# Optimization experiments

Measured on AMD Instinct MI355X. Metric: run time of the kernel, lower is better.

## Reference

```python
import jax, jax.numpy as jnp
import numpy as np

L, B, E, H, NH = 128, 32, 128, 256, 8
NUM_NODE, ETA = 20000, 100


def setup_inputs() -> dict:
    key = jax.random.key(0)
    ks = jax.random.split(key, 24)
    s = 0.05
    rn = lambda k, sh: jax.random.normal(k, sh, dtype=jnp.float32) * s
    return {
        "node": jax.random.randint(ks[0], (L, B), 0, NUM_NODE + 1),
        "ts": jax.random.normal(ks[1], (L, B, 2), dtype=jnp.float32),
        "seq_lengths": jnp.sort(jax.random.randint(ks[2], (B,), 64, L + 1))[::-1],
        "embed_table": rn(ks[3], (NUM_NODE + 1, E)),
        "Wih0": rn(ks[4], (3 * H, E + 2)), "Whh0": rn(ks[5], (3 * H, H)),
        "bih0": rn(ks[6], (3 * H,)), "bhh0": rn(ks[7], (3 * H,)),
        "Wih1": rn(ks[8], (3 * H, H)), "Whh1": rn(ks[9], (3 * H, H)),
        "bih1": rn(ks[10], (3 * H,)), "bhh1": rn(ks[11], (3 * H,)),
        "Wa0": rn(ks[12], (E, 2 * E)), "ba0": rn(ks[13], (E,)),
        "Wa1": rn(ks[14], (NH, E)), "ba1": rn(ks[15], (NH,)),
        "Wf0": rn(ks[16], (168, H * (NH + 1))), "bf0": rn(ks[17], (168,)),
        "Wf1": rn(ks[18], (ETA, 168)), "bf1": rn(ks[19], (ETA,)),
    }


def gru_layer(x, Wih, Whh, bih, bhh, lengths):
    # x: [L, B, in]; PyTorch GRU cell, with pack/pad semantics:
    # hidden frozen and output zeroed for t >= length (emulates pack_padded_sequence).
    Lx, Bx, _ = x.shape

    def step(h, xs):
        x_t, t = xs
        gi = x_t @ Wih.T + bih          # [B, 3H]
        gh = h @ Whh.T + bhh            # [B, 3H]
        ir, iz, in_ = jnp.split(gi, 3, axis=-1)
        hr, hz, hn = jnp.split(gh, 3, axis=-1)
        r = jax.nn.sigmoid(ir + hr)
        z = jax.nn.sigmoid(iz + hz)
        n = jnp.tanh(in_ + r * hn)
        h_new = (1.0 - z) * n + z * h
        valid = (t < lengths)[:, None]
        h = jnp.where(valid, h_new, h)
        return h, jnp.where(valid, h_new, jnp.zeros_like(h_new))

    h0 = jnp.zeros((Bx, Whh.shape[1]), x.dtype)
    hT, outs = jax.lax.scan(step, h0, (x, jnp.arange(Lx)))
    return outs, hT


def reference(node, ts, seq_lengths, embed_table,
              Wih0, Whh0, bih0, bhh0, Wih1, Whh1, bih1, bhh1,
              Wa0, ba0, Wa1, ba1, Wf0, bf0, Wf1, bf1):
    e = embed_table[node]                          # [L, B, E]
    embeds = jnp.concatenate([e, ts], axis=-1)     # [L, B, E+2]

    # pairwise attention: a[i,j] = e[j], b[i,j] = e[i] (repeat + transpose)
    a = jnp.broadcast_to(e[None], (L, L, B, E))
    b = jnp.broadcast_to(e[:, None], (L, L, B, E))
    pair = jnp.concatenate([a, b], axis=-1)        # [L, L, B, 2E]
    hid = jax.nn.relu(pair @ Wa0.T + ba0)          # [L, L, B, E]
    w = (hid @ Wa1.T + ba1).sum(axis=1)            # [L, B, NH]

    # multiplicative length mask, then softmax over time axis (as in original)
    mask = (jnp.arange(L)[:, None] < seq_lengths[None, :]).astype(w.dtype)[..., None]
    w = jax.nn.softmax(w * mask, axis=0)           # [L, B, NH]

    out0, _ = gru_layer(embeds, Wih0, Whh0, bih0, bhh0, seq_lengths)
    out1, hT = gru_layer(out0, Wih1, Whh1, bih1, bhh1, seq_lengths)  # [L,B,H], [B,H]

    ctx = jnp.einsum('lbh,lbd->bhd', w, out1).reshape(B, NH * H)     # [B, NH*H]
    z = jnp.concatenate([ctx, hT], axis=-1) @ Wf0.T + bf0
    z = jax.nn.selu(z)
    logits = z @ Wf1.T + bf1
    return jax.nn.log_softmax(logits, axis=-1)
```

## Files before the change

kernel.cpp:

```cpp
#include <hip/hip_runtime.h>
#include <hip/hip_bf16.h>

#define LL 128
#define BB 32
#define EE 128
#define HH 256
#define NHH 8
#define G3 768
#define IN0 130
#define ETA 100
#define F1 168
#define CLSIN 2304

typedef _Float16 half_t;
typedef __attribute__((ext_vector_type(2))) _Float16 half2v;
typedef __attribute__((ext_vector_type(8))) _Float16 f16x8;
typedef __attribute__((ext_vector_type(4))) float f32x4;

#if defined(__has_builtin)
#if __has_builtin(__builtin_amdgcn_fdot2)
#define HAVE_FDOT2 1
#endif
#endif

__device__ __forceinline__ float fdot2f(half2v a, half2v b, float c) {
#ifdef HAVE_FDOT2
  return __builtin_amdgcn_fdot2(a, b, c, false);
#else
  return c + (float)a.x * (float)b.x + (float)a.y * (float)b.y;
#endif
}

#define BARRIER_LDS() __asm__ volatile("s_waitcnt lgkmcnt(0)\n\ts_barrier" ::: "memory")

__device__ __forceinline__ float sigmoidf_(float x) { return 1.0f / (1.0f + __expf(-x)); }
__device__ __forceinline__ float tanhf_(float x) { return 1.0f - 2.0f / (__expf(2.0f * x) + 1.0f); }

__global__ void prep_kernel(
    const float* __restrict__ Wa0, const float* __restrict__ Wih0,
    const float* __restrict__ Wih1, const float* __restrict__ Whh0,
    const float* __restrict__ Whh1,
    half_t* __restrict__ Wa0Ta, half_t* __restrict__ Wa0Tb,
    half2v* __restrict__ Wih0T2, half2v* __restrict__ Wih1T2,
    half_t* __restrict__ Whh0h, half_t* __restrict__ Whh1h)
{
  int idx = blockIdx.x * blockDim.x + threadIdx.x;
  const int n1 = 16384, n2 = 16384, n3 = 65 * 768, n4 = 128 * 768, n5 = 196608;
  if (idx < n1) {
    int d = idx >> 7, k = idx & 127;
    Wa0Ta[idx] = (half_t)Wa0[k * 256 + d];
  } else if ((idx -= n1) < n2) {
    int d = idx >> 7, k = idx & 127;
    Wa0Tb[idx] = (half_t)Wa0[k * 256 + 128 + d];
  } else if ((idx -= n2) < n3) {
    int d2 = idx / 768, r = idx % 768;
    half2v w; w.x = (half_t)Wih0[r * IN0 + 2 * d2]; w.y = (half_t)Wih0[r * IN0 + 2 * d2 + 1];
    Wih0T2[idx] = w;
  } else if ((idx -= n3) < n4) {
    int d2 = idx / 768, r = idx % 768;
    half2v w; w.x = (half_t)Wih1[r * HH + 2 * d2]; w.y = (half_t)Wih1[r * HH + 2 * d2 + 1];
    Wih1T2[idx] = w;
  } else if ((idx -= n4) < n5) {
    Whh0h[idx] = (half_t)Whh0[idx];
  } else if ((idx -= n5) < n5) {
    Whh1h[idx] = (half_t)Whh1[idx];
  }
}

__global__ void embed_uv_kernel(
    const int* __restrict__ node,
    const float* __restrict__ table,
    const half_t* __restrict__ Wa0Ta,
    const half_t* __restrict__ Wa0Tb,
    const float* __restrict__ ba0,
    half2v* __restrict__ e_h2,
    float* __restrict__ U,
    float* __restrict__ V)
{
  int lb = blockIdx.x;
  int k = threadIdx.x;
  __shared__ float es[EE];
  int n = node[lb];
  float ev = table[(size_t)n * EE + k];
  es[k] = ev;
  __syncthreads();
  if (k < 64) {
    half2v p; p.x = (half_t)es[2 * k]; p.y = (half_t)es[2 * k + 1];
    e_h2[(size_t)lb * 64 + k] = p;
  }
  float u = 0.f, v = ba0[k];
  #pragma unroll 8
  for (int d = 0; d < EE; ++d) {
    float x = es[d];
    u += (float)Wa0Ta[d * EE + k] * x;
    v += (float)Wa0Tb[d * EE + k] * x;
  }
  U[(size_t)lb * EE + k] = u;
  V[(size_t)lb * EE + k] = v;
}

__global__ __launch_bounds__(128) void attn_w_kernel(
    const float* __restrict__ U, const float* __restrict__ V,
    const float* __restrict__ Wa1,
    const float* __restrict__ ba1,
    float* __restrict__ wpre)
{
  int ig = blockIdx.x >> 5;
  int b = blockIdx.x & 31;
  int i0 = ig * 4;
  int k = threadIdx.x;
  float vk[4];
  #pragma unroll
  for (int ii = 0; ii < 4; ++ii) vk[ii] = V[((size_t)(i0 + ii) * BB + b) * EE + k];
  float wa[NHH], acc[4][NHH];
  #pragma unroll
  for (int h = 0; h < NHH; ++h) wa[h] = Wa1[h * EE + k];
  #pragma unroll
  for (int ii = 0; ii < 4; ++ii)
    #pragma unroll
    for (int h = 0; h < NHH; ++h) acc[ii][h] = 0.f;
  for (int j = 0; j < LL; ++j) {
    float u = U[((size_t)j * BB + b) * EE + k];
    #pragma unroll
    for (int ii = 0; ii < 4; ++ii) {
      float tv = fmaxf(u + vk[ii], 0.f);
      #pragma unroll
      for (int h = 0; h < NHH; ++h) acc[ii][h] += wa[h] * tv;
    }
  }
  __shared__ float part[2][32];
  int wave = k >> 6, lane = k & 63;
  #pragma unroll
  for (int ii = 0; ii < 4; ++ii)
    #pragma unroll
    for (int h = 0; h < NHH; ++h) {
      float a = acc[ii][h];
      #pragma unroll
      for (int off = 32; off > 0; off >>= 1) a += __shfl_xor(a, off, 64);
      if (lane == 0) part[wave][ii * 8 + h] = a;
    }
  __syncthreads();
  if (k < 32) {
    int ii = k >> 3, h = k & 7;
    float w = part[0][k] + part[1][k] + (float)LL * ba1[h];
    wpre[((size_t)(i0 + ii) * BB + b) * NHH + h] = w;
  }
}

__global__ void attn_softmax_kernel(
    const float* __restrict__ wpre, const int* __restrict__ slen,
    float* __restrict__ wsoft)
{
  int b = blockIdx.x >> 3;
  int h = blockIdx.x & 7;
  int l = threadIdx.x;
  int len = slen[b];
  float x = wpre[((size_t)l * BB + b) * NHH + h];
  float xv = (l < len) ? x : 0.f;
  float m = xv;
  #pragma unroll
  for (int off = 32; off > 0; off >>= 1) m = fmaxf(m, __shfl_xor(m, off, 64));
  __shared__ float sm[2], ss[2];
  int wave = l >> 6;
  if ((l & 63) == 0) sm[wave] = m;
  __syncthreads();
  m = fmaxf(sm[0], sm[1]);
  float e = __expf(xv - m);
  float s = e;
  #pragma unroll
  for (int off = 32; off > 0; off >>= 1) s += __shfl_xor(s, off, 64);
  if ((l & 63) == 0) ss[wave] = s;
  __syncthreads();
  s = ss[0] + ss[1];
  wsoft[((size_t)l * BB + b) * NHH + h] = e / s;
}

__global__ __launch_bounds__(256) void gi0_kernel(
    const half2v* __restrict__ e_h2, const float* __restrict__ ts,
    const half2v* __restrict__ W2,
    const float* __restrict__ bih,
    const float* __restrict__ bhh,
    float* __restrict__ gi)
{
  int lb0 = blockIdx.x * 8;
  int tid = threadIdx.x;
  __shared__ half2v xs2[8][66];
  for (int idx = tid; idx < 512; idx += 256) {
    int q = idx >> 6, d2 = idx & 63;
    xs2[q][d2] = e_h2[(size_t)(lb0 + q) * 64 + d2];
  }
  if (tid < 8) {
    half2v t2; t2.x = (half_t)ts[(lb0 + tid) * 2]; t2.y = (half_t)ts[(lb0 + tid) * 2 + 1];
    xs2[tid][64] = t2;
  }
  __syncthreads();
  float acc[8][3];
  #pragma unroll
  for (int q = 0; q < 8; ++q) { acc[q][0] = 0.f; acc[q][1] = 0.f; acc[q][2] = 0.f; }
  for (int d2 = 0; d2 < 65; ++d2) {
    half2v w0 = W2[d2 * 768 + tid];
    half2v w1 = W2[d2 * 768 + 256 + tid];
    half2v w2 = W2[d2 * 768 + 512 + tid];
    #pragma unroll
    for (int q = 0; q < 8; ++q) {
      half2v x = xs2[q][d2];
      acc[q][0] = fdot2f(w0, x, acc[q][0]);
      acc[q][1] = fdot2f(w1, x, acc[q][1]);
      acc[q][2] = fdot2f(w2, x, acc[q][2]);
    }
  }
  float b0 = bih[tid] + bhh[tid];
  float b1 = bih[256 + tid] + bhh[256 + tid];
  float b2 = bih[512 + tid];
  #pragma unroll
  for (int q = 0; q < 8; ++q) {
    float* gp = gi + (size_t)(lb0 + q) * G3;
    gp[tid] = acc[q][0] + b0; gp[256 + tid] = acc[q][1] + b1; gp[512 + tid] = acc[q][2] + b2;
  }
}

__global__ __launch_bounds__(256) void gi1_kernel(
    const float* __restrict__ out0,
    const half2v* __restrict__ W2,
    const float* __restrict__ bih,
    const float* __restrict__ bhh,
    float* __restrict__ gi)
{
  int lb0 = blockIdx.x * 8;
  int tid = threadIdx.x;
  __shared__ half2v xs2[8][128];
  for (int idx = tid; idx < 1024; idx += 256) {
    int q = idx >> 7, d2 = idx & 127;
    float2 v = ((const float2*)(out0 + (size_t)(lb0 + q) * HH))[d2];
    half2v x; x.x = (half_t)v.x; x.y = (half_t)v.y;
    xs2[q][d2] = x;
  }
  __syncthreads();
  float acc[8][3];
  #pragma unroll
  for (int q = 0; q < 8; ++q) { acc[q][0] = 0.f; acc[q][1] = 0.f; acc[q][2] = 0.f; }
  for (int d2 = 0; d2 < 128; ++d2) {
    half2v w0 = W2[d2 * 768 + tid];
    half2v w1 = W2[d2 * 768 + 256 + tid];
    half2v w2 = W2[d2 * 768 + 512 + tid];
    #pragma unroll
    for (int q = 0; q < 8; ++q) {
      half2v x = xs2[q][d2];
      acc[q][0] = fdot2f(w0, x, acc[q][0]);
      acc[q][1] = fdot2f(w1, x, acc[q][1]);
      acc[q][2] = fdot2f(w2, x, acc[q][2]);
    }
  }
  float b0 = bih[tid] + bhh[tid];
  float b1 = bih[256 + tid] + bhh[256 + tid];
  float b2 = bih[512 + tid];
  #pragma unroll
  for (int q = 0; q < 8; ++q) {
    float* gp = gi + (size_t)(lb0 + q) * G3;
    gp[tid] = acc[q][0] + b0; gp[256 + tid] = acc[q][1] + b1; gp[512 + tid] = acc[q][2] + b2;
  }
}

__global__ __launch_bounds__(256, 1) void gru_scan_kernel(
    const half_t* __restrict__ Whhh,
    const float* __restrict__ bhh,
    const float* __restrict__ gi,
    const int* __restrict__ slen,
    float* __restrict__ out,
    float* __restrict__ hT)
{
  const int b = blockIdx.x;
  const int tid = threadIdx.x;
  const int w = tid >> 6;
  const int lane = tid & 63;
  const int m = lane & 15;
  const int kg = lane >> 4;

  __shared__ __align__(16) half_t hbuf[2][HH];
  __shared__ __align__(16) float gsum[G3];

  f16x8 A[96];
  #pragma unroll
  for (int g = 0; g < 3; ++g)
    #pragma unroll
    for (int j = 0; j < 4; ++j) {
      int row = (g << 8) + (w << 6) + (j << 4) + m;
      const half_t* wb = Whhh + (size_t)row * HH + kg * 8;
      #pragma unroll
      for (int kc = 0; kc < 8; ++kc)
        A[(g * 4 + j) * 8 + kc] = *(const f16x8*)(wb + kc * 32);
    }

  const int len = slen[b];
  const float bhn = bhh[2 * HH + tid];
  float hold = 0.f;
  hbuf[0][tid] = (half_t)0.f;
  hbuf[1][tid] = (half_t)0.f;
  __syncthreads();

  const float* gib = gi + (size_t)b * G3;
  float* outb = out + (size_t)b * HH;

  #pragma unroll 1
  for (int t = 0; t < LL; ++t) {
    const int p = t & 1;
    const float* gp = gib + (size_t)t * (BB * G3);
    float g0 = gp[tid], g1 = gp[HH + tid], g2 = gp[2 * HH + tid];
    f16x8 bf[8];
    #pragma unroll
    for (int kc = 0; kc < 8; ++kc)
      bf[kc] = *(const f16x8*)&hbuf[p][kc * 32 + kg * 8];
    f32x4 C[12];
    #pragma unroll
    for (int tl = 0; tl < 12; ++tl) C[tl] = (f32x4){0.f, 0.f, 0.f, 0.f};
    #pragma unroll
    for (int kc = 0; kc < 8; ++kc)
      #pragma unroll
      for (int tl = 0; tl < 12; ++tl)
        C[tl] = __builtin_amdgcn_mfma_f32_16x16x32_f16(A[tl * 8 + kc], bf[kc], C[tl], 0, 0, 0);
    if (m == 0) {
      #pragma unroll
      for (int g = 0; g < 3; ++g)
        #pragma unroll
        for (int j = 0; j < 4; ++j)
          *(f32x4*)&gsum[(g << 8) + (w << 6) + (j << 4) + (kg << 2)] = C[g * 4 + j];
    }
    BARRIER_LDS();
    {
      float r_ = sigmoidf_(g0 + gsum[tid]);
      float z_ = sigmoidf_(g1 + gsum[HH + tid]);
      float n_ = tanhf_(g2 + r_ * (gsum[2 * HH + tid] + bhn));
      float hnew = (1.f - z_) * n_ + z_ * hold;
      bool valid = t < len;
      hold = valid ? hnew : hold;
      hbuf[p ^ 1][tid] = (half_t)hold;
      outb[(size_t)t * (BB * HH) + tid] = valid ? hnew : 0.f;
    }
    BARRIER_LDS();
  }
  hT[(size_t)b * HH + tid] = hold;
}

__global__ void ctx_kernel(
    const float* __restrict__ wsoft, const float* __restrict__ out1,
    float* __restrict__ ctx)
{
  int b = blockIdx.x >> 3, h = blockIdx.x & 7;
  int d = threadIdx.x;
  float acc = 0.f;
  for (int l = 0; l < LL; ++l) {
    float w = wsoft[((size_t)l * BB + b) * NHH + h];
    acc += w * out1[((size_t)l * BB + b) * HH + d];
  }
  ctx[(size_t)b * (NHH * HH) + h * HH + d] = acc;
}

__global__ __launch_bounds__(512) void final_kernel(
    const float* __restrict__ ctx, const float* __restrict__ hT,
    const float* __restrict__ Wf0,
    const float* __restrict__ bf0,
    const float* __restrict__ Wf1,
    const float* __restrict__ bf1,
    float* __restrict__ outp)
{
  int b = blockIdx.x;
  int tid = threadIdx.x;
  int wave = tid >> 6, lane = tid & 63;
  __shared__ float4 xs4[CLSIN / 4];
  __shared__ float zs[F1];
  __shared__ float ls[ETA];
  float* xs = (float*)xs4;
  for (int i = tid; i < NHH * HH; i += 512) xs[i] = ctx[(size_t)b * (NHH * HH) + i];
  if (tid < HH) xs[NHH * HH + tid] = hT[(size_t)b * HH + tid];
  __syncthreads();
  for (int r = wave; r < F1; r += 8) {
    const float4* wp = (const float4*)(Wf0 + (size_t)r * CLSIN);
    float acc = 0.f;
    #pragma unroll
    for (int i = 0; i < CLSIN / 4 / 64; ++i) {
      float4 w = wp[lane + 64 * i];
      float4 x = xs4[lane + 64 * i];
      acc += w.x * x.x + w.y * x.y + w.z * x.z + w.w * x.w;
    }
    #pragma unroll
    for (int off = 32; off > 0; off >>= 1) acc += __shfl_xor(acc, off, 64);
    if (lane == 0) {
      float x = acc + bf0[r];
      const float alpha = 1.6732632423543772f, scale = 1.0507009873554805f;
      zs[r] = scale * (x > 0.f ? x : alpha * (__expf(x) - 1.f));
    }
  }
  __syncthreads();
  for (int r = wave; r < ETA; r += 8) {
    float acc = 0.f;
    for (int k = lane; k < F1; k += 64) acc += Wf1[r * F1 + k] * zs[k];
    #pragma unroll
    for (int off = 32; off > 0; off >>= 1) acc += __shfl_xor(acc, off, 64);
    if (lane == 0) ls[r] = acc + bf1[r];
  }
  __syncthreads();
  if (wave == 0) {
    float v0 = (lane < ETA) ? ls[lane] : -1e30f;
    float v1 = (lane + 64 < ETA) ? ls[lane + 64] : -1e30f;
    float m = fmaxf(v0, v1);
    #pragma unroll
    for (int off = 32; off > 0; off >>= 1) m = fmaxf(m, __shfl_xor(m, off, 64));
    float s = __expf(v0 - m) + __expf(v1 - m);
    #pragma unroll
    for (int off = 32; off > 0; off >>= 1) s += __shfl_xor(s, off, 64);
    float lse = m + __logf(s);
    if (lane < ETA) outp[(size_t)b * ETA + lane] = v0 - lse;
    if (lane + 64 < ETA) outp[(size_t)b * ETA + lane + 64] = v1 - lse;
  }
}

extern "C" void kernel_launch(void* const* d_in, const int* in_sizes, int n_in,
                              void* d_out, int out_size, void* d_ws, size_t ws_size,
                              hipStream_t stream) {
  const int*   node  = (const int*)d_in[0];
  const float* ts    = (const float*)d_in[1];
  const int*   slen  = (const int*)d_in[2];
  const float* table = (const float*)d_in[3];
  const float* Wih0  = (const float*)d_in[4];
  const float* Whh0  = (const float*)d_in[5];
  const float* bih0  = (const float*)d_in[6];
  const float* bhh0  = (const float*)d_in[7];
  const float* Wih1  = (const float*)d_in[8];
  const float* Whh1  = (const float*)d_in[9];
  const float* bih1  = (const float*)d_in[10];
  const float* bhh1  = (const float*)d_in[11];
  const float* Wa0   = (const float*)d_in[12];
  const float* ba0   = (const float*)d_in[13];
  const float* Wa1   = (const float*)d_in[14];
  const float* ba1   = (const float*)d_in[15];
  const float* Wf0   = (const float*)d_in[16];
  const float* bf0   = (const float*)d_in[17];
  const float* Wf1   = (const float*)d_in[18];
  const float* bf1   = (const float*)d_in[19];

  char* ws = (char*)d_ws;
  size_t off = 0;
  auto alloc = [&](size_t n) { void* p = (void*)(ws + off); off += (n + 255) & ~(size_t)255; return p; };

  half2v* e_h2 = (half2v*)alloc((size_t)LL * BB * 64 * 4);
  float* U     = (float*)alloc((size_t)LL * BB * EE * 4);
  float* V     = (float*)alloc((size_t)LL * BB * EE * 4);
  float* gi    = (float*)alloc((size_t)LL * BB * G3 * 4);
  float* out0  = (float*)alloc((size_t)LL * BB * HH * 4);
  float* out1  = (float*)alloc((size_t)LL * BB * HH * 4);
  float* hTb   = (float*)alloc((size_t)BB * HH * 4);
  float* wpre  = (float*)alloc((size_t)LL * BB * NHH * 4);
  float* wsoft = (float*)alloc((size_t)LL * BB * NHH * 4);
  float* ctxb  = (float*)alloc((size_t)BB * NHH * HH * 4);
  half_t* Wa0Ta = (half_t*)alloc((size_t)128 * 128 * 2);
  half_t* Wa0Tb = (half_t*)alloc((size_t)128 * 128 * 2);
  half2v* Wih0T2 = (half2v*)alloc((size_t)65 * 768 * 4);
  half2v* Wih1T2 = (half2v*)alloc((size_t)128 * 768 * 4);
  half_t* Whh0h = (half_t*)alloc((size_t)G3 * HH * 2);
  half_t* Whh1h = (half_t*)alloc((size_t)G3 * HH * 2);
  if (off > ws_size) return;

  const int prep_total = 16384 + 16384 + 65 * 768 + 128 * 768 + 196608 + 196608;
  prep_kernel<<<(prep_total + 255) / 256, 256, 0, stream>>>(
      Wa0, Wih0, Wih1, Whh0, Whh1, Wa0Ta, Wa0Tb, Wih0T2, Wih1T2, Whh0h, Whh1h);
  embed_uv_kernel<<<LL * BB, 128, 0, stream>>>(node, table, Wa0Ta, Wa0Tb, ba0, e_h2, U, V);
  attn_w_kernel<<<(LL / 4) * BB, 128, 0, stream>>>(U, V, Wa1, ba1, wpre);
  attn_softmax_kernel<<<BB * NHH, 128, 0, stream>>>(wpre, slen, wsoft);
  gi0_kernel<<<LL * BB / 8, 256, 0, stream>>>(e_h2, ts, Wih0T2, bih0, bhh0, gi);
  gru_scan_kernel<<<BB, 256, 0, stream>>>(Whh0h, bhh0, gi, slen, out0, hTb);
  gi1_kernel<<<LL * BB / 8, 256, 0, stream>>>(out0, Wih1T2, bih1, bhh1, gi);
  gru_scan_kernel<<<BB, 256, 0, stream>>>(Whh1h, bhh1, gi, slen, out1, hTb);
  ctx_kernel<<<BB * NHH, 256, 0, stream>>>(wsoft, out1, ctxb);
  final_kernel<<<BB, 512, 0, stream>>>(ctxb, hTb, Wf0, bf0, Wf1, bf1, (float*)d_out);
}
```

Before: 707.6 us.

## Replace MFMA recurrent GEMV with per-thread fdot2 rows over 768 threads

The GRU scan kernel now uses 768 threads per batch block. Each thread keeps one full fp16 row of Whh in registers (128 packed uints) and computes its gate dot product with packed fdot2, reading h from LDS as broadcast vector loads. This replaces the 256-thread MFMA formulation, which computed 16x16 tiles where only one column held useful data (a matrix-vector product). The aim is to shorten the per-step latency of the serial recurrence. The cost is much higher register pressure per thread, a serial dependent chain of 128 fdot2 ops split into two accumulators, and idle threads in the gate update phase.

```diff
diff --git a/kernel.cpp b/kernel.cpp
--- a/kernel.cpp
+++ b/kernel.cpp
@@ -14,8 +14,7 @@
 
 typedef _Float16 half_t;
 typedef __attribute__((ext_vector_type(2))) _Float16 half2v;
-typedef __attribute__((ext_vector_type(8))) _Float16 f16x8;
-typedef __attribute__((ext_vector_type(4))) float f32x4;
+typedef __attribute__((ext_vector_type(16))) unsigned int uint16v;
 
 #if defined(__has_builtin)
 #if __has_builtin(__builtin_amdgcn_fdot2)
@@ -29,6 +28,9 @@
 #else
   return c + (float)a.x * (float)b.x + (float)a.y * (float)b.y;
 #endif
+}
+__device__ __forceinline__ float fdot2u(unsigned int a, unsigned int b, float c) {
+  return fdot2f(__builtin_bit_cast(half2v, a), __builtin_bit_cast(half2v, b), c);
 }
 
 #define BARRIER_LDS() __asm__ volatile("s_waitcnt lgkmcnt(0)\n\ts_barrier" ::: "memory")
@@ -261,7 +263,7 @@
   }
 }
 
-__global__ __launch_bounds__(256, 1) void gru_scan_kernel(
+__global__ __launch_bounds__(768, 3) void gru_scan_kernel(
     const half_t* __restrict__ Whhh,
     const float* __restrict__ bhh,
     const float* __restrict__ gi,
@@ -271,31 +273,30 @@
 {
   const int b = blockIdx.x;
   const int tid = threadIdx.x;
-  const int w = tid >> 6;
-  const int lane = tid & 63;
-  const int m = lane & 15;
-  const int kg = lane >> 4;
-
   __shared__ __align__(16) half_t hbuf[2][HH];
-  __shared__ __align__(16) float gsum[G3];
-
-  f16x8 A[96];
-  #pragma unroll
-  for (int g = 0; g < 3; ++g)
-    #pragma unroll
-    for (int j = 0; j < 4; ++j) {
-      int row = (g << 8) + (w << 6) + (j << 4) + m;
-      const half_t* wb = Whhh + (size_t)row * HH + kg * 8;
-      #pragma unroll
-      for (int kc = 0; kc < 8; ++kc)
-        A[(g * 4 + j) * 8 + kc] = *(const f16x8*)(wb + kc * 32);
-    }
+  __shared__ float gsum[G3];
+
+  uint16v W[8];
+  {
+    const uint4* wp = (const uint4*)(Whhh + (size_t)tid * HH);
+    #pragma unroll
+    for (int j = 0; j < 32; ++j) {
+      uint4 v = wp[j];
+      int base = 4 * j;
+      W[base >> 4][(base & 15) + 0] = v.x;
+      W[base >> 4][(base & 15) + 1] = v.y;
+      W[base >> 4][(base & 15) + 2] = v.z;
+      W[base >> 4][(base & 15) + 3] = v.w;
+    }
+  }
 
   const int len = slen[b];
-  const float bhn = bhh[2 * HH + tid];
-  float hold = 0.f;
-  hbuf[0][tid] = (half_t)0.f;
-  hbuf[1][tid] = (half_t)0.f;
+  float bhn = 0.f, hold = 0.f;
+  if (tid < HH) {
+    bhn = bhh[2 * HH + tid];
+    hbuf[0][tid] = (half_t)0.f;
+    hbuf[1][tid] = (half_t)0.f;
+  }
   __syncthreads();
 
   const float* gib = gi + (size_t)b * G3;
@@ -304,29 +305,36 @@
   #pragma unroll 1
   for (int t = 0; t < LL; ++t) {
     const int p = t & 1;
-    const float* gp = gib + (size_t)t * (BB * G3);
-    float g0 = gp[tid], g1 = gp[HH + tid], g2 = gp[2 * HH + tid];
-    f16x8 bf[8];
-    #pragma unroll
-    for (int kc = 0; kc < 8; ++kc)
-      bf[kc] = *(const f16x8*)&hbuf[p][kc * 32 + kg * 8];
-    f32x4 C[12];
-    #pragma unroll
-    for (int tl = 0; tl < 12; ++tl) C[tl] = (f32x4){0.f, 0.f, 0.f, 0.f};
-    #pragma unroll
-    for (int kc = 0; kc < 8; ++kc)
-      #pragma unroll
-      for (int tl = 0; tl < 12; ++tl)
-        C[tl] = __builtin_amdgcn_mfma_f32_16x16x32_f16(A[tl * 8 + kc], bf[kc], C[tl], 0, 0, 0);
-    if (m == 0) {
-      #pragma unroll
-      for (int g = 0; g < 3; ++g)
-        #pragma unroll
-        for (int j = 0; j < 4; ++j)
-          *(f32x4*)&gsum[(g << 8) + (w << 6) + (j << 4) + (kg << 2)] = C[g * 4 + j];
-    }
+    float g0 = 0.f, g1 = 0.f, g2 = 0.f;
+    if (tid < HH) {
+      const float* gp = gib + (size_t)t * (BB * G3);
+      g0 = gp[tid]; g1 = gp[HH + tid]; g2 = gp[2 * HH + tid];
+    }
+    float accA = 0.f, accB = 0.f;
+    const uint4* hb = (const uint4*)hbuf[p];
+    #pragma unroll
+    for (int j = 0; j < 32; ++j) {
+      uint4 hc = hb[j];
+      int i0 = 4 * j;
+      unsigned int w0 = W[i0 >> 4][(i0 & 15) + 0];
+      unsigned int w1 = W[i0 >> 4][(i0 & 15) + 1];
+      unsigned int w2 = W[i0 >> 4][(i0 & 15) + 2];
+      unsigned int w3 = W[i0 >> 4][(i0 & 15) + 3];
+      if (j & 1) {
+        accB = fdot2u(w0, hc.x, accB);
+        accB = fdot2u(w1, hc.y, accB);
+        accB = fdot2u(w2, hc.z, accB);
+        accB = fdot2u(w3, hc.w, accB);
+      } else {
+        accA = fdot2u(w0, hc.x, accA);
+        accA = fdot2u(w1, hc.y, accA);
+        accA = fdot2u(w2, hc.z, accA);
+        accA = fdot2u(w3, hc.w, accA);
+      }
+    }
+    gsum[tid] = accA + accB;
     BARRIER_LDS();
-    {
+    if (tid < HH) {
       float r_ = sigmoidf_(g0 + gsum[tid]);
       float z_ = sigmoidf_(g1 + gsum[HH + tid]);
       float n_ = tanhf_(g2 + r_ * (gsum[2 * HH + tid] + bhn));
@@ -338,7 +346,7 @@
     }
     BARRIER_LDS();
   }
-  hT[(size_t)b * HH + tid] = hold;
+  if (tid < HH) hT[(size_t)b * HH + tid] = hold;
 }
 
 __global__ void ctx_kernel(
@@ -467,9 +475,9 @@
   attn_w_kernel<<<(LL / 4) * BB, 128, 0, stream>>>(U, V, Wa1, ba1, wpre);
   attn_softmax_kernel<<<BB * NHH, 128, 0, stream>>>(wpre, slen, wsoft);
   gi0_kernel<<<LL * BB / 8, 256, 0, stream>>>(e_h2, ts, Wih0T2, bih0, bhh0, gi);
-  gru_scan_kernel<<<BB, 256, 0, stream>>>(Whh0h, bhh0, gi, slen, out0, hTb);
+  gru_scan_kernel<<<BB, 768, 0, stream>>>(Whh0h, bhh0, gi, slen, out0, hTb);
   gi1_kernel<<<LL * BB / 8, 256, 0, stream>>>(out0, Wih1T2, bih1, bhh1, gi);
-  gru_scan_kernel<<<BB, 256, 0, stream>>>(Whh1h, bhh1, gi, slen, out1, hTb);
+  gru_scan_kernel<<<BB, 768, 0, stream>>>(Whh1h, bhh1, gi, slen, out1, hTb);
   ctx_kernel<<<BB * NHH, 256, 0, stream>>>(wsoft, out1, ctxb);
   final_kernel<<<BB, 512, 0, stream>>>(ctxb, hTb, Wf0, bf0, Wf1, bf1, (float*)d_out);
 }
```

New measurement: 624.6 us. 11.7% less time.

## Batch 16 sequences per GRU scan block using MFMA N dimension

Applied to the files above, without the earlier changes.

The GRU recurrent scan moves from one block per batch element (32 blocks of 256 threads, matvec with only one useful MFMA column) to two blocks of 512 threads, each handling 16 batch elements as the MFMA N dimension. Each wave holds half as many weight tiles, and gate math is done directly from the MFMA accumulators in registers, so the gsum LDS round trip and one barrier per step go away. The cost is that only 2 CUs run the scan, each doing 16x more useful MFMA work per step, and the hidden state is now kept in both fp32 and fp16 LDS buffers.

```diff
diff --git a/kernel.cpp b/kernel.cpp
--- a/kernel.cpp
+++ b/kernel.cpp
@@ -14,6 +14,7 @@
 
 typedef _Float16 half_t;
 typedef __attribute__((ext_vector_type(2))) _Float16 half2v;
+typedef __attribute__((ext_vector_type(4))) _Float16 half4v;
 typedef __attribute__((ext_vector_type(8))) _Float16 f16x8;
 typedef __attribute__((ext_vector_type(4))) float f32x4;
 
@@ -261,7 +262,7 @@
   }
 }
 
-__global__ __launch_bounds__(256, 1) void gru_scan_kernel(
+__global__ __launch_bounds__(512, 2) void gru_scan_kernel(
     const half_t* __restrict__ Whhh,
     const float* __restrict__ bhh,
     const float* __restrict__ gi,
@@ -269,76 +270,83 @@
     float* __restrict__ out,
     float* __restrict__ hT)
 {
-  const int b = blockIdx.x;
+  const int bi = blockIdx.x;
   const int tid = threadIdx.x;
   const int w = tid >> 6;
   const int lane = tid & 63;
   const int m = lane & 15;
   const int kg = lane >> 4;
 
-  __shared__ __align__(16) half_t hbuf[2][HH];
-  __shared__ __align__(16) float gsum[G3];
-
-  f16x8 A[96];
+  __shared__ __align__(16) half_t HT[2][16][264];
+  __shared__ __align__(16) float  H32[2][16][260];
+
+  f16x8 A[48];
   #pragma unroll
   for (int g = 0; g < 3; ++g)
     #pragma unroll
-    for (int j = 0; j < 4; ++j) {
-      int row = (g << 8) + (w << 6) + (j << 4) + m;
+    for (int j = 0; j < 2; ++j) {
+      int row = (g << 8) + (w << 5) + (j << 4) + m;
       const half_t* wb = Whhh + (size_t)row * HH + kg * 8;
       #pragma unroll
       for (int kc = 0; kc < 8; ++kc)
-        A[(g * 4 + j) * 8 + kc] = *(const f16x8*)(wb + kc * 32);
-    }
-
-  const int len = slen[b];
-  const float bhn = bhh[2 * HH + tid];
-  float hold = 0.f;
-  hbuf[0][tid] = (half_t)0.f;
-  hbuf[1][tid] = (half_t)0.f;
-  __syncthreads();
-
-  const float* gib = gi + (size_t)b * G3;
-  float* outb = out + (size_t)b * HH;
+        A[(g * 2 + j) * 8 + kc] = *(const f16x8*)(wb + kc * 32);
+    }
+
+  const int u0base = (w << 5) + (kg << 2);
+  const int lenv = slen[bi * 16 + m];
+  f32x4 bhn4[2];
+  #pragma unroll
+  for (int j = 0; j < 2; ++j)
+    bhn4[j] = *(const f32x4*)(bhh + 2 * HH + u0base + (j << 4));
+
+  for (int i = tid; i < 16 * 264; i += 512) ((half_t*)HT[0])[i] = (half_t)0.f;
+  for (int i = tid; i < 16 * 260; i += 512) ((float*)H32[0])[i] = 0.f;
+  __syncthreads();
 
   #pragma unroll 1
   for (int t = 0; t < LL; ++t) {
     const int p = t & 1;
-    const float* gp = gib + (size_t)t * (BB * G3);
-    float g0 = gp[tid], g1 = gp[HH + tid], g2 = gp[2 * HH + tid];
-    f16x8 bf[8];
-    #pragma unroll
-    for (int kc = 0; kc < 8; ++kc)
-      bf[kc] = *(const f16x8*)&hbuf[p][kc * 32 + kg * 8];
-    f32x4 C[12];
-    #pragma unroll
-    for (int tl = 0; tl < 12; ++tl) C[tl] = (f32x4){0.f, 0.f, 0.f, 0.f};
-    #pragma unroll
-    for (int kc = 0; kc < 8; ++kc)
+    f32x4 C[6];
+    #pragma unroll
+    for (int tl = 0; tl < 6; ++tl) C[tl] = (f32x4){0.f, 0.f, 0.f, 0.f};
+    #pragma unroll
+    for (int kc = 0; kc < 8; ++kc) {
+      f16x8 bf = *(const f16x8*)&HT[p][m][kc * 32 + kg * 8];
       #pragma unroll
-      for (int tl = 0; tl < 12; ++tl)
-        C[tl] = __builtin_amdgcn_mfma_f32_16x16x32_f16(A[tl * 8 + kc], bf[kc], C[tl], 0, 0, 0);
-    if (m == 0) {
+      for (int tl = 0; tl < 6; ++tl)
+        C[tl] = __builtin_amdgcn_mfma_f32_16x16x32_f16(A[tl * 8 + kc], bf, C[tl], 0, 0, 0);
+    }
+    const float* gb = gi + (size_t)t * (BB * G3) + (size_t)(bi * 16 + m) * G3 + u0base;
+    const bool valid = t < lenv;
+    #pragma unroll
+    for (int j = 0; j < 2; ++j) {
+      f32x4 gr = *(const f32x4*)(gb + (j << 4));
+      f32x4 gz = *(const f32x4*)(gb + HH + (j << 4));
+      f32x4 gn = *(const f32x4*)(gb + 2 * HH + (j << 4));
+      int u0 = u0base + (j << 4);
+      f32x4 ho = *(const f32x4*)&H32[p][m][u0];
+      f32x4 hs, o4; half4v hv;
       #pragma unroll
-      for (int g = 0; g < 3; ++g)
-        #pragma unroll
-        for (int j = 0; j < 4; ++j)
-          *(f32x4*)&gsum[(g << 8) + (w << 6) + (j << 4) + (kg << 2)] = C[g * 4 + j];
+      for (int r = 0; r < 4; ++r) {
+        float rr = sigmoidf_(gr[r] + C[j][r]);
+        float zz = sigmoidf_(gz[r] + C[2 + j][r]);
+        float nn = tanhf_(gn[r] + rr * (C[4 + j][r] + bhn4[j][r]));
+        float hnew = (1.f - zz) * nn + zz * ho[r];
+        float hst = valid ? hnew : ho[r];
+        hs[r] = hst;
+        o4[r] = valid ? hnew : 0.f;
+        hv[r] = (half_t)hst;
+      }
+      *(f32x4*)&H32[p ^ 1][m][u0] = hs;
+      *(half4v*)&HT[p ^ 1][m][u0] = hv;
+      *(f32x4*)(out + (size_t)t * (BB * HH) + (size_t)(bi * 16 + m) * HH + u0) = o4;
     }
     BARRIER_LDS();
-    {
-      float r_ = sigmoidf_(g0 + gsum[tid]);
-      float z_ = sigmoidf_(g1 + gsum[HH + tid]);
-      float n_ = tanhf_(g2 + r_ * (gsum[2 * HH + tid] + bhn));
-      float hnew = (1.f - z_) * n_ + z_ * hold;
-      bool valid = t < len;
-      hold = valid ? hnew : hold;
-      hbuf[p ^ 1][tid] = (half_t)hold;
-      outb[(size_t)t * (BB * HH) + tid] = valid ? hnew : 0.f;
-    }
-    BARRIER_LDS();
-  }
-  hT[(size_t)b * HH + tid] = hold;
+  }
+  for (int idx = tid; idx < 16 * HH; idx += 512) {
+    int mm = idx >> 8, uu = idx & 255;
+    hT[(size_t)(bi * 16 + mm) * HH + uu] = H32[0][mm][uu];
+  }
 }
 
 __global__ void ctx_kernel(
@@ -467,9 +475,9 @@
   attn_w_kernel<<<(LL / 4) * BB, 128, 0, stream>>>(U, V, Wa1, ba1, wpre);
   attn_softmax_kernel<<<BB * NHH, 128, 0, stream>>>(wpre, slen, wsoft);
   gi0_kernel<<<LL * BB / 8, 256, 0, stream>>>(e_h2, ts, Wih0T2, bih0, bhh0, gi);
-  gru_scan_kernel<<<BB, 256, 0, stream>>>(Whh0h, bhh0, gi, slen, out0, hTb);
+  gru_scan_kernel<<<2, 512, 0, stream>>>(Whh0h, bhh0, gi, slen, out0, hTb);
   gi1_kernel<<<LL * BB / 8, 256, 0, stream>>>(out0, Wih1T2, bih1, bhh1, gi);
-  gru_scan_kernel<<<BB, 256, 0, stream>>>(Whh1h, bhh1, gi, slen, out1, hTb);
+  gru_scan_kernel<<<2, 512, 0, stream>>>(Whh1h, bhh1, gi, slen, out1, hTb);
   ctx_kernel<<<BB * NHH, 256, 0, stream>>>(wsoft, out1, ctxb);
   final_kernel<<<BB, 512, 0, stream>>>(ctxb, hTb, Wf0, bf0, Wf1, bf1, (float*)d_out);
 }
```

After: 1.368 ms. +93.3%, slower.
